# Kernel optimization log

Measured on AMD Instinct MI355X. Metric: run time of the kernel, lower is better.

Reference implementation:

```python
import jax, jax.numpy as jnp
import numpy as np

B, S, A, H1, H2, N = 32768, 512, 8, 400, 300, 3
P = 0.1          # dropout_p
NOISE_VAR = 1e-4  # _noise_variance
INV_SQRT2 = 0.7071067811865476
INV_SQRT2PI = 0.3989422804014327


def adf_relu(m, v):
    # ADF ReLU moment matching (Gast & Roth style, as in adf.ReLU)
    std = jnp.sqrt(v)
    r = m / std
    cdf = 0.5 * (1.0 + jax.lax.erf(r * INV_SQRT2))
    pdf = INV_SQRT2PI * jnp.exp(-0.5 * r * r)
    om = m * cdf + std * pdf
    ov = (m * m + v) * cdf + m * std * pdf - om * om
    return om, ov


def setup_inputs():
    key = jax.random.key(0)
    ks = jax.random.split(key, 10)
    x = jax.random.normal(ks[0], (B, S), jnp.float32)
    x_noise = jax.random.normal(ks[1], (B, S), jnp.float32)
    v1 = 10.0 / np.sqrt(S)   # fanin_init for linear1
    W1 = jax.random.uniform(ks[2], (H1, S), jnp.float32, -v1, v1)
    b1 = jax.random.uniform(ks[3], (H1,), jnp.float32, -1.0 / np.sqrt(S), 1.0 / np.sqrt(S))
    v2 = 10.0 / np.sqrt(H1)  # fanin_init for linear2
    W2 = jax.random.uniform(ks[4], (H2, H1), jnp.float32, -v2, v2)
    b2 = jax.random.uniform(ks[5], (H2,), jnp.float32, -1.0 / np.sqrt(H1), 1.0 / np.sqrt(H1))
    W3 = jax.random.uniform(ks[6], (A, H2), jnp.float32, -0.003, 0.003)
    b3 = jax.random.uniform(ks[7], (A,), jnp.float32, -0.003, 0.003)
    # MC-dropout masks for dropout_n=3 iterations, values in {0, 1/(1-p)}
    mask1 = jax.random.bernoulli(ks[8], 1.0 - P, (N, B, H1)).astype(jnp.float32) / (1.0 - P)
    mask2 = jax.random.bernoulli(ks[9], 1.0 - P, (N, B, H2)).astype(jnp.float32) / (1.0 - P)
    return dict(x=x, x_noise=x_noise, W1=W1, b1=b1, W2=W2, b2=b2, W3=W3, b3=b3,
                mask1=mask1, mask2=mask2)


def reference(x, x_noise, W1, b1, W2, b2, W3, b3, mask1, mask2):
    # input variance: _noise_variance + 2 (constant)
    var0 = jnp.full_like(x, NOISE_VAR + 2.0)
    # global min-max normalize mean, then +0.1
    mn = (x - x.min()) / (x.max() - x.min()) + 0.1
    # linear1 + ADF ReLU are deterministic: compute once, broadcast to N samples
    m = mn @ W1.T + b1              # [B,H1]
    v = var0 @ (W1 * W1).T          # [B,H1]
    m, v = adf_relu(m, v)
    m = m[None] * mask1             # [N,B,H1]
    v = v[None] * (mask1 * mask1)
    m = m @ W2.T + b2               # [N,B,H2]
    v = v @ (W2 * W2).T
    m, v = adf_relu(m, v)
    m = m * mask2
    v = v * (mask2 * mask2)
    m = m @ W3.T + b3               # [N,B,A]
    v = v @ (W3 * W3).T
    mean_out = m.mean(0)            # [B,A]
    # mean of ADF variances + empirical variance of MC means
    var_out = v.mean(0) + ((mean_out[None] - m) ** 2).mean(0)
    var_out = 10.0 ** var_out       # elementwise math.pow(10, .)
    return mean_out, var_out
```

## Files before the change

kernel.cpp:

```cpp
#include <hip/hip_runtime.h>


typedef unsigned short u16;
typedef unsigned int u32;
typedef float f32x4 __attribute__((ext_vector_type(4)));
typedef __bf16 bf16x8 __attribute__((ext_vector_type(8)));
typedef u32 u32x4 __attribute__((ext_vector_type(4)));

union U4 { u32x4 u; bf16x8 v; u16 s[8]; };

#define MFMA16(a, b, c) __builtin_amdgcn_mfma_f32_16x16x32_bf16(a, b, c, 0, 0, 0)

#define B_N 32768
#define S_N 512
#define H1_N 400
#define H2_N 300
#define A_N 8

__device__ __forceinline__ float bf2f(u16 h) {
    union { float f; u32 u; } c; c.u = ((u32)h) << 16; return c.f;
}
__device__ __forceinline__ u16 f2bfbits(float f) {
    union { __bf16 h; u16 u; } c; c.h = (__bf16)f; return c.u;
}
__device__ __forceinline__ u32 encf(float f) {
    u32 u = __float_as_uint(f);
    return (u & 0x80000000u) ? ~u : (u | 0x80000000u);
}
__device__ __forceinline__ float decf(u32 e) {
    u32 u = (e >> 31) ? (e & 0x7FFFFFFFu) : ~e;
    return __uint_as_float(u);
}

__device__ __forceinline__ void adf_relu(float m, float v, float& om, float& ov) {
    v = fmaxf(v, 1e-12f);
    float rstd = rsqrtf(v);
    float stdv = v * rstd;
    float r = m * rstd;
    float e = __expf(-0.5f * r * r);
    float ar = fabsf(r) * 0.70710678118654752f;
    float t = __builtin_amdgcn_rcpf(fmaf(0.3275911f, ar, 1.0f));
    float poly = t * (0.254829592f + t * (-0.284496736f + t * (1.421413741f +
                  t * (-1.453152027f + t * 1.061405429f))));
    float erfa = 1.0f - poly * e;
    float erfv = (r < 0.0f) ? -erfa : erfa;
    float cdf = 0.5f * (1.0f + erfv);
    float pdf = 0.3989422804014327f * e;
    om = fmaf(m, cdf, stdv * pdf);
    ov = fmaf(m * m + v, cdf, m * stdv * pdf) - om * om;
    ov = fmaxf(ov, 0.0f);
}

#define WS_CTL    0u
#define WS_B1F    64u
#define WS_B2F    1664u
#define WS_B3F    2880u
#define WS_RS1    2944u
#define WS_VC1    4544u
#define WS_W3M    6144u
#define WS_W3V    16384u
#define WS_W2SQ   26624u
#define WS_W2B    266624u
#define WS_W1B    506624u
#define WS_OMOV   916224u
#define WS_MP     53345024u
#define WS_VP     56490752u

__global__ void k_detect(const u32* __restrict__ xw, u32* __restrict__ ctl) {
    if (threadIdx.x == 0) {
        int votes = 0;
        for (int i = 0; i < 64; ++i) {
            u32 u = xw[i * 997];
            u32 e = (u >> 7) & 0xFFu;
            votes += (e >= 100u && e <= 145u) ? 1 : 0;
        }
        ctl[0] = (votes >= 40) ? 1u : 0u;
        ctl[1] = 0xFFFFFFFFu;
        ctl[2] = 0u;
    }
}

__global__ void k_weights(const void* __restrict__ w1r, const void* __restrict__ w2r,
                          const void* __restrict__ w3r, const void* __restrict__ b1r,
                          const void* __restrict__ b2r, const void* __restrict__ b3r,
                          const u32* __restrict__ ctl,
                          u16* __restrict__ w1b, u16* __restrict__ w2b,
                          u16* __restrict__ w2sq, u16* __restrict__ w3m,
                          u16* __restrict__ w3v, float* __restrict__ b1f,
                          float* __restrict__ b2f, float* __restrict__ b3f) {
    const bool bf = ctl[0] != 0u;
    const int t = blockIdx.x * 256 + threadIdx.x;

    if (t < (H2_N * H1_N / 8)) {
        float f[8];
        if (bf) {
            U4 d; d.u = *(const u32x4*)((const u16*)w2r + (size_t)t * 8);
            #pragma unroll
            for (int j = 0; j < 8; ++j) f[j] = bf2f(d.s[j]);
        } else {
            f32x4 a = *((const f32x4*)w2r + (size_t)t * 2);
            f32x4 b = *((const f32x4*)w2r + (size_t)t * 2 + 1);
            #pragma unroll
            for (int j = 0; j < 4; ++j) { f[j] = a[j]; f[4 + j] = b[j]; }
        }
        u16 sq[8], cv[8];
        #pragma unroll
        for (int j = 0; j < 8; ++j) { sq[j] = f2bfbits(f[j] * f[j]); cv[j] = f2bfbits(f[j]); }
        *(u32x4*)(w2sq + (size_t)t * 8) = *(u32x4*)sq;
        if (!bf) *(u32x4*)(w2b + (size_t)t * 8) = *(u32x4*)cv;
    }
    if (!bf && t < (H1_N * S_N / 8)) {
        f32x4 a = *((const f32x4*)w1r + (size_t)t * 2);
        f32x4 b = *((const f32x4*)w1r + (size_t)t * 2 + 1);
        u16 cv[8];
        #pragma unroll
        for (int j = 0; j < 4; ++j) { cv[j] = f2bfbits(a[j]); cv[4 + j] = f2bfbits(b[j]); }
        *(u32x4*)(w1b + (size_t)t * 8) = *(u32x4*)cv;
    }
    if (t < 16 * 320) {
        int col = t / 320, k = t - col * 320;
        float f = 0.0f;
        if (col < A_N && k < H2_N)
            f = bf ? bf2f(((const u16*)w3r)[col * H2_N + k]) : ((const float*)w3r)[col * H2_N + k];
        w3m[t] = f2bfbits(f);
        w3v[t] = f2bfbits(f * f);
    }
    if (t < H1_N) b1f[t] = bf ? bf2f(((const u16*)b1r)[t]) : ((const float*)b1r)[t];
    if (t < H2_N) b2f[t] = bf ? bf2f(((const u16*)b2r)[t]) : ((const float*)b2r)[t];
    if (t < A_N)  b3f[t] = bf ? bf2f(((const u16*)b3r)[t]) : ((const float*)b3r)[t];
}

__global__ void k_minmax(const void* __restrict__ xr, u32* __restrict__ ctl) {
    const int tid = threadIdx.x, lane = tid & 63, wv = tid >> 6;
    const bool bf = ctl[0] != 0u;
    float mn = 3.0e38f, mx = -3.0e38f;
    const int idx = blockIdx.x * 256 + tid;
    if (bf) {
        const u16* xg = (const u16*)xr;
        for (int i = idx; i < (B_N * S_N / 8); i += 2048 * 256) {
            U4 d; d.u = *(const u32x4*)(xg + (size_t)i * 8);
            #pragma unroll
            for (int j = 0; j < 8; ++j) {
                float f = bf2f(d.s[j]);
                mn = fminf(mn, f); mx = fmaxf(mx, f);
            }
        }
    } else {
        const f32x4* xf = (const f32x4*)xr;
        for (int i = idx; i < (B_N * S_N / 4); i += 2048 * 256) {
            f32x4 d = xf[i];
            #pragma unroll
            for (int j = 0; j < 4; ++j) {
                mn = fminf(mn, d[j]); mx = fmaxf(mx, d[j]);
            }
        }
    }
    #pragma unroll
    for (int off = 32; off >= 1; off >>= 1) {
        mn = fminf(mn, __shfl_xor(mn, off));
        mx = fmaxf(mx, __shfl_xor(mx, off));
    }
    __shared__ float rmn[4], rmx[4];
    if (lane == 0) { rmn[wv] = mn; rmx[wv] = mx; }
    __syncthreads();
    if (tid == 0) {
        for (int w = 1; w < 4; ++w) { mn = fminf(mn, rmn[w]); mx = fmaxf(mx, rmx[w]); }
        atomicMin(&ctl[1], encf(mn));
        atomicMax(&ctl[2], encf(mx));
    }
}

__global__ void k_prep(const void* __restrict__ w1r, const u32* __restrict__ ctl,
                       float* __restrict__ rs1, float* __restrict__ vc1) {
    const bool bf = ctl[0] != 0u;
    const int h = blockIdx.x, lane = threadIdx.x;
    float f[8];
    if (bf) {
        U4 d; d.u = *(const u32x4*)((const u16*)w1r + (size_t)h * S_N + lane * 8);
        #pragma unroll
        for (int j = 0; j < 8; ++j) f[j] = bf2f(d.s[j]);
    } else {
        f32x4 a = *((const f32x4*)w1r + (size_t)h * 128 + lane * 2);
        f32x4 b = *((const f32x4*)w1r + (size_t)h * 128 + lane * 2 + 1);
        #pragma unroll
        for (int j = 0; j < 4; ++j) { f[j] = a[j]; f[4 + j] = b[j]; }
    }
    float s1 = 0.f, s2 = 0.f;
    #pragma unroll
    for (int j = 0; j < 8; ++j) { s1 += f[j]; s2 += f[j] * f[j]; }
    #pragma unroll
    for (int off = 32; off >= 1; off >>= 1) {
        s1 += __shfl_xor(s1, off);
        s2 += __shfl_xor(s2, off);
    }
    if (lane == 0) { rs1[h] = s1; vc1[h] = 2.0001f * s2; }
}

__global__ __launch_bounds__(256, 4)
void k_l1(const void* __restrict__ xr, const u16* __restrict__ w1bf,
          const u16* __restrict__ w1cv, const float* __restrict__ b1f,
          const float* __restrict__ rs1, const float* __restrict__ vc1,
          const u32* __restrict__ ctl, u32* __restrict__ omovg) {
    const int tid = threadIdx.x, wv = tid >> 6, lane = tid & 63;
    const int lrow = lane & 15, lgrp = lane >> 4;
    const int m0 = blockIdx.x * 128;
    const int n0 = blockIdx.y * 112;
    const bool bf = ctl[0] != 0u;
    const u16* w1 = bf ? w1bf : w1cv;
    const float xmin = decf(ctl[1]), xmax = decf(ctl[2]);
    const float inv = 1.0f / (xmax - xmin);
    const float csh = 0.1f - xmin * inv;

    const f32x4 fz = {0.f, 0.f, 0.f, 0.f};
    f32x4 acc[2][7];
    #pragma unroll
    for (int i = 0; i < 2; ++i)
        #pragma unroll
        for (int j = 0; j < 7; ++j) acc[i][j] = fz;

    const int rowA = m0 + wv * 32 + lrow;
    if (bf) {
        const u16* xg = (const u16*)xr;
        const size_t ar0 = (size_t)rowA * S_N + lgrp * 8;
        const size_t ar1 = ar0 + (size_t)16 * S_N;
        U4 nx0, nx1;
        nx0.u = *(const u32x4*)(xg + ar0);
        nx1.u = *(const u32x4*)(xg + ar1);
        for (int ks = 0; ks < 16; ++ks) {
            U4 a0 = nx0, a1 = nx1;
            if (ks < 15) {
                nx0.u = *(const u32x4*)(xg + ar0 + (ks + 1) * 32);
                nx1.u = *(const u32x4*)(xg + ar1 + (ks + 1) * 32);
            }
            const int k = ks * 32 + lgrp * 8;
            #pragma unroll
            for (int ct = 0; ct < 7; ++ct) {
                const int col = n0 + ct * 16 + lrow;
                U4 b; b.u = 0;
                if (col < H1_N) b.u = *(const u32x4*)(w1 + (size_t)col * S_N + k);
                acc[0][ct] = MFMA16(a0.v, b.v, acc[0][ct]);
                acc[1][ct] = MFMA16(a1.v, b.v, acc[1][ct]);
            }
        }
    } else {
        const f32x4* xf = (const f32x4*)xr;
        const size_t q0 = ((size_t)rowA * S_N + lgrp * 8) >> 2;
        const size_t q1 = q0 + (size_t)16 * S_N / 4;
        f32x4 n0a = xf[q0], n0b = xf[q0 + 1], n1a = xf[q1], n1b = xf[q1 + 1];
        for (int ks = 0; ks < 16; ++ks) {
            f32x4 c0a = n0a, c0b = n0b, c1a = n1a, c1b = n1b;
            if (ks < 15) {
                const size_t o = (size_t)(ks + 1) * 8;
                n0a = xf[q0 + o]; n0b = xf[q0 + o + 1];
                n1a = xf[q1 + o]; n1b = xf[q1 + o + 1];
            }
            U4 a0, a1;
            #pragma unroll
            for (int j = 0; j < 4; ++j) {
                a0.s[j] = f2bfbits(c0a[j]); a0.s[4 + j] = f2bfbits(c0b[j]);
                a1.s[j] = f2bfbits(c1a[j]); a1.s[4 + j] = f2bfbits(c1b[j]);
            }
            const int k = ks * 32 + lgrp * 8;
            #pragma unroll
            for (int ct = 0; ct < 7; ++ct) {
                const int col = n0 + ct * 16 + lrow;
                U4 b; b.u = 0;
                if (col < H1_N) b.u = *(const u32x4*)(w1 + (size_t)col * S_N + k);
                acc[0][ct] = MFMA16(a0.v, b.v, acc[0][ct]);
                acc[1][ct] = MFMA16(a1.v, b.v, acc[1][ct]);
            }
        }
    }
    #pragma unroll
    for (int ct = 0; ct < 7; ++ct) {
        const int col = n0 + ct * 16 + lrow;
        if (col < H1_N) {
            const float c1 = csh * rs1[col] + b1f[col];
            const float vv = vc1[col];
            #pragma unroll
            for (int r2 = 0; r2 < 2; ++r2)
                #pragma unroll
                for (int r = 0; r < 4; ++r) {
                    const int row = m0 + wv * 32 + r2 * 16 + lgrp * 4 + r;
                    float mm = fmaf(inv, acc[r2][ct][r], c1);
                    float omx, ovx; adf_relu(mm, vv, omx, ovx);
                    omovg[(size_t)row * H1_N + col] =
                        (u32)f2bfbits(omx) | ((u32)f2bfbits(ovx) << 16);
                }
        }
    }
}

__global__ __launch_bounds__(256, 3)
void k_l23(const u32* __restrict__ omovg, const u16* __restrict__ w2bf,
           const u16* __restrict__ w2cv, const u16* __restrict__ w2sqg,
           const void* __restrict__ m1r, const void* __restrict__ m2r,
           const float* __restrict__ b2f,
           const u16* __restrict__ w3mg, const u16* __restrict__ w3vg,
           const u32* __restrict__ ctl, float* __restrict__ mpart,
           float* __restrict__ vpart) {
    __shared__ __align__(16) unsigned char smem[52224];
    u16* pmS = (u16*)smem;
    u16* pvS = (u16*)(smem + 26112);
    u16* m2s = (u16*)smem;
    u16* v2s = (u16*)(smem + 26112);

    const int tid = threadIdx.x;
    const int wv = tid >> 6, lane = tid & 63;
    const int lrow = lane & 15, lgrp = lane >> 4;
    const int bx = blockIdx.x;
    const int n = bx % 3;
    const int m0 = (bx / 3) * 32;
    const bool bf = ctl[0] != 0u;
    const u16* w2 = bf ? w2bf : w2cv;
    const f32x4 fz = {0.f, 0.f, 0.f, 0.f};

    #pragma unroll 2
    for (int p = 0; p < 7; ++p) {
        const int c = tid + p * 256;
        if (c < 1600) {
            const int row = c / 50, kc = (c - row * 50) * 8;
            const size_t base = (size_t)(m0 + row) * H1_N + kc;
            u32x4 o0 = *(const u32x4*)(omovg + base);
            u32x4 o1 = *(const u32x4*)(omovg + base + 4);
            const size_t mb = ((size_t)n * B_N + m0 + row) * H1_N + kc;
            u32x4 k0 = {0, 0, 0, 0}, k1 = {0, 0, 0, 0};
            if (bf) {
                k0 = *(const u32x4*)((const u16*)m1r + mb);
            } else {
                k0 = *(const u32x4*)((const float*)m1r + mb);
                k1 = *(const u32x4*)((const float*)m1r + mb + 4);
            }
            u16 pm[8], pv[8];
            #pragma unroll
            for (int j = 0; j < 8; ++j) {
                const u32 w = (j < 4) ? o0[j] : o1[j - 4];
                const float omf = __uint_as_float(w << 16);
                const float ovf = __uint_as_float(w & 0xFFFF0000u);
                float mf;
                if (bf) {
                    const u32 mw = k0[j >> 1];
                    mf = bf2f((u16)((j & 1) ? (mw >> 16) : (mw & 0xFFFFu)));
                } else {
                    mf = __uint_as_float((j < 4) ? k0[j] : k1[j - 4]);
                }
                pm[j] = f2bfbits(omf * mf);
                pv[j] = f2bfbits(ovf * mf * mf);
            }
            *(u32x4*)(pmS + row * 408 + kc) = *(u32x4*)pm;
            *(u32x4*)(pvS + row * 408 + kc) = *(u32x4*)pv;
        }
    }
    __syncthreads();

    f32x4 accM[2][5], accV[2][5];
    #pragma unroll
    for (int i = 0; i < 2; ++i)
        #pragma unroll
        for (int j = 0; j < 5; ++j) { accM[i][j] = fz; accV[i][j] = fz; }

    #pragma unroll 1
    for (int ks = 0; ks < 12; ++ks) {
        const int k0 = ks * 32;
        bf16x8 amf[2], avf[2];
        #pragma unroll
        for (int r2 = 0; r2 < 2; ++r2) {
            const int idx = (r2 * 16 + lrow) * 408 + k0 + lgrp * 8;
            amf[r2] = *(const bf16x8*)(pmS + idx);
            avf[r2] = *(const bf16x8*)(pvS + idx);
        }
        const int kb = k0 + lgrp * 8;
        #pragma unroll
        for (int ct = 0; ct < 5; ++ct) {
            const int col = wv * 80 + ct * 16 + lrow;
            U4 bm, bv; bm.u = 0; bv.u = 0;
            if (col < H2_N) {
                const size_t bidx = (size_t)col * H1_N + kb;
                bm.u = *(const u32x4*)(w2 + bidx);
                bv.u = *(const u32x4*)(w2sqg + bidx);
            }
            accM[0][ct] = MFMA16(amf[0], bm.v, accM[0][ct]);
            accM[1][ct] = MFMA16(amf[1], bm.v, accM[1][ct]);
            accV[0][ct] = MFMA16(avf[0], bv.v, accV[0][ct]);
            accV[1][ct] = MFMA16(avf[1], bv.v, accV[1][ct]);
        }
    }
    {
        const bool kv = lgrp < 2;
        const int ko = kv ? lgrp * 8 : 0;
        bf16x8 amf[2], avf[2];
        #pragma unroll
        for (int r2 = 0; r2 < 2; ++r2) {
            const int idx = (r2 * 16 + lrow) * 408 + 384 + ko;
            U4 ta, tv;
            ta.v = *(const bf16x8*)(pmS + idx);
            tv.v = *(const bf16x8*)(pvS + idx);
            if (!kv) { ta.u = 0; tv.u = 0; }
            amf[r2] = ta.v; avf[r2] = tv.v;
        }
        const int kb = 384 + lgrp * 8;
        #pragma unroll
        for (int ct = 0; ct < 5; ++ct) {
            const int col = wv * 80 + ct * 16 + lrow;
            U4 bm, bv; bm.u = 0; bv.u = 0;
            if (col < H2_N && kb < H1_N) {
                const size_t bidx = (size_t)col * H1_N + kb;
                bm.u = *(const u32x4*)(w2 + bidx);
                bv.u = *(const u32x4*)(w2sqg + bidx);
            }
            accM[0][ct] = MFMA16(amf[0], bm.v, accM[0][ct]);
            accM[1][ct] = MFMA16(amf[1], bm.v, accM[1][ct]);
            accV[0][ct] = MFMA16(avf[0], bv.v, accV[0][ct]);
            accV[1][ct] = MFMA16(avf[1], bv.v, accV[1][ct]);
        }
    }
    __syncthreads();

    float msk[2][5][4];
    #pragma unroll
    for (int r2 = 0; r2 < 2; ++r2)
        #pragma unroll
        for (int ct = 0; ct < 5; ++ct) {
            const int col = wv * 80 + ct * 16 + lrow;
            #pragma unroll
            for (int r = 0; r < 4; ++r) {
                const int rl = r2 * 16 + lgrp * 4 + r;
                float mf = 0.0f;
                if (col < H2_N) {
                    const size_t midx = ((size_t)n * B_N + m0 + rl) * H2_N + col;
                    mf = bf ? bf2f(((const u16*)m2r)[midx])
                            : ((const float*)m2r)[midx];
                }
                msk[r2][ct][r] = mf;
            }
        }

    #pragma unroll
    for (int r2 = 0; r2 < 2; ++r2)
        #pragma unroll
        for (int ct = 0; ct < 5; ++ct) {
            const int col = wv * 80 + ct * 16 + lrow;
            const float b2v = (col < H2_N) ? b2f[col] : 0.0f;
            #pragma unroll
            for (int r = 0; r < 4; ++r) {
                const int rl = r2 * 16 + lgrp * 4 + r;
                u16 wm = 0, wvs = 0;
                if (col < H2_N) {
                    float mm = accM[r2][ct][r] + b2v;
                    float vvx = accV[r2][ct][r];
                    float omx, ovx; adf_relu(mm, vvx, omx, ovx);
                    const float mskv = msk[r2][ct][r];
                    wm  = f2bfbits(omx * mskv);
                    wvs = f2bfbits(ovx * mskv * mskv);
                }
                m2s[rl * 328 + col] = wm;
                v2s[rl * 328 + col] = wvs;
            }
        }
    __syncthreads();

    {
        const int typ = wv & 1, rt = wv >> 1;
        const u16* slab = typ ? v2s : m2s;
        const u16* w3t  = typ ? w3vg : w3mg;
        f32x4 c3 = fz;
        #pragma unroll
        for (int kk = 0; kk < 10; ++kk) {
            const int aidx = (rt * 16 + lrow) * 328 + kk * 32 + lgrp * 8;
            bf16x8 af = *(const bf16x8*)(slab + aidx);
            U4 bw; bw.u = *(const u32x4*)(w3t + (size_t)lrow * 320 + kk * 32 + lgrp * 8);
            c3 = MFMA16(af, bw.v, c3);
        }
        float* part = typ ? vpart : mpart;
        if (lrow < A_N) {
            #pragma unroll
            for (int r = 0; r < 4; ++r) {
                const int rl = rt * 16 + lgrp * 4 + r;
                part[((size_t)n * B_N + m0 + rl) * 8 + lrow] = c3[r];
            }
        }
    }
}

__global__ __launch_bounds__(256)
void k_out(const float* __restrict__ mpart, const float* __restrict__ vpart,
           const float* __restrict__ b3f, const u32* __restrict__ ctl,
           void* __restrict__ outr) {
    const size_t idx = (size_t)blockIdx.x * 256 + threadIdx.x;
    const int a = (int)(idx & 7);
    const size_t st = (size_t)B_N * 8;
    const float m0 = mpart[idx], m1 = mpart[st + idx], m2 = mpart[2 * st + idx];
    const float v0 = vpart[idx], v1 = vpart[st + idx], v2 = vpart[2 * st + idx];
    const float md = (m0 + m1 + m2) * (1.0f / 3.0f);
    const float sm2 = (m0 * m0 + m1 * m1 + m2 * m2) * (1.0f / 3.0f);
    const float meanout = md + b3f[a];
    const float vexp = (v0 + v1 + v2) * (1.0f / 3.0f) + sm2 - md * md;
    const float varout = __expf(vexp * 2.302585092994046f);
    const bool bf = ctl[0] != 0u;
    if (bf) {
        ((u16*)outr)[idx] = f2bfbits(meanout);
        ((u16*)outr)[st + idx] = f2bfbits(varout);
    } else {
        ((float*)outr)[idx] = meanout;
        ((float*)outr)[st + idx] = varout;
    }
}

extern "C" void kernel_launch(void* const* d_in, const int* in_sizes, int n_in,
                              void* d_out, int out_size, void* d_ws, size_t ws_size,
                              hipStream_t stream) {
    const void* x     = d_in[0];
    const void* W1    = d_in[2];
    const void* b1    = d_in[3];
    const void* W2    = d_in[4];
    const void* b2    = d_in[5];
    const void* W3    = d_in[6];
    const void* b3    = d_in[7];
    const void* mask1 = d_in[8];
    const void* mask2 = d_in[9];

    char* ws = (char*)d_ws;
    u32*   ctl   = (u32*)(ws + WS_CTL);
    float* b1f   = (float*)(ws + WS_B1F);
    float* b2f   = (float*)(ws + WS_B2F);
    float* b3f   = (float*)(ws + WS_B3F);
    float* rs1   = (float*)(ws + WS_RS1);
    float* vc1   = (float*)(ws + WS_VC1);
    u16*   w3m   = (u16*)(ws + WS_W3M);
    u16*   w3v   = (u16*)(ws + WS_W3V);
    u16*   w2sq  = (u16*)(ws + WS_W2SQ);
    u16*   w2b   = (u16*)(ws + WS_W2B);
    u16*   w1b   = (u16*)(ws + WS_W1B);
    u32*   omov  = (u32*)(ws + WS_OMOV);
    float* mpart = (float*)(ws + WS_MP);
    float* vpart = (float*)(ws + WS_VP);

    k_detect<<<1, 64, 0, stream>>>((const u32*)x, ctl);
    k_weights<<<100, 256, 0, stream>>>(W1, W2, W3, b1, b2, b3, ctl,
                                       w1b, w2b, w2sq, w3m, w3v, b1f, b2f, b3f);
    k_minmax<<<2048, 256, 0, stream>>>(x, ctl);
    k_prep<<<400, 64, 0, stream>>>(W1, ctl, rs1, vc1);
    k_l1<<<dim3(256, 4), 256, 0, stream>>>(x, (const u16*)W1, w1b, b1f, rs1, vc1,
                                           ctl, omov);
    k_l23<<<3072, 256, 0, stream>>>(omov, (const u16*)W2, w2b, w2sq, mask1, mask2,
                                    b2f, w3m, w3v, ctl, mpart, vpart);
    k_out<<<1024, 256, 0, stream>>>(mpart, vpart, b3f, ctl, d_out);
}
```

Baseline: 658.3 us.

## Compress dropout masks to bitmaps and scale by a single global mask constant

Adds a pre-pass kernel that reads both dropout masks once and packs them into per-element bitmaps. It also ORs all mask bit patterns together to recover the single nonzero scale value. The layer-1 epilogue folds that scale into the stored mean and variance. The layer-2/3 kernel then reads compact bit bytes instead of full float or bf16 masks, replacing the scattered per-element mask2 loads. The OR trick assumes every nonzero mask entry has the same value, and the bitmap path runs only when the workspace is large enough.

```diff
diff --git a/kernel.cpp b/kernel.cpp
--- a/kernel.cpp
+++ b/kernel.cpp
@@ -6,6 +6,7 @@
 typedef float f32x4 __attribute__((ext_vector_type(4)));
 typedef __bf16 bf16x8 __attribute__((ext_vector_type(8)));
 typedef u32 u32x4 __attribute__((ext_vector_type(4)));
+typedef u32 u32x2 __attribute__((ext_vector_type(2)));
 
 union U4 { u32x4 u; bf16x8 v; u16 s[8]; };
 
@@ -65,6 +66,8 @@
 #define WS_OMOV   916224u
 #define WS_MP     53345024u
 #define WS_VP     56490752u
+#define WS_BM1    59636480u
+#define WS_BM2    64551680u
 
 __global__ void k_detect(const u32* __restrict__ xw, u32* __restrict__ ctl) {
     if (threadIdx.x == 0) {
@@ -77,6 +80,94 @@
         ctl[0] = (votes >= 40) ? 1u : 0u;
         ctl[1] = 0xFFFFFFFFu;
         ctl[2] = 0u;
+        ctl[3] = 0u;
+        ctl[4] = 0u;
+    }
+}
+
+__global__ __launch_bounds__(256)
+void k_mcomp(const void* __restrict__ m1r, const void* __restrict__ m2r,
+             u32* __restrict__ ctl, unsigned char* __restrict__ bm1,
+             unsigned char* __restrict__ bm2) {
+    const bool bf = ctl[0] != 0u;
+    const int bid = blockIdx.x;
+    u32 orv = 0;
+    if (bid < 2400) {
+        const int t = bid * 256 + threadIdx.x;
+        const size_t e0 = (size_t)t * 64;
+        u32 b0 = 0, b1 = 0;
+        if (bf) {
+            #pragma unroll
+            for (int v = 0; v < 8; ++v) {
+                u32x4 d = *(const u32x4*)((const u16*)m1r + e0 + v * 8);
+                #pragma unroll
+                for (int j = 0; j < 4; ++j) {
+                    const u32 w = d[j];
+                    orv |= (w << 16) | (w & 0xFFFF0000u);
+                    const int e = v * 8 + j * 2;
+                    if (w & 0xFFFFu) { if (e < 32) b0 |= 1u << e; else b1 |= 1u << (e - 32); }
+                    if (w >> 16) { if (e + 1 < 32) b0 |= 1u << (e + 1); else b1 |= 1u << (e - 31); }
+                }
+            }
+        } else {
+            #pragma unroll
+            for (int v = 0; v < 16; ++v) {
+                u32x4 d = *(const u32x4*)((const u32*)m1r + e0 + v * 4);
+                #pragma unroll
+                for (int j = 0; j < 4; ++j) {
+                    const u32 w = d[j];
+                    orv |= w;
+                    const int e = v * 4 + j;
+                    if (w) { if (e < 32) b0 |= 1u << e; else b1 |= 1u << (e - 32); }
+                }
+            }
+        }
+        u32x2 bb = {b0, b1};
+        *(u32x2*)(bm1 + (size_t)t * 8) = bb;
+        #pragma unroll
+        for (int off = 32; off >= 1; off >>= 1) orv |= __shfl_xor(orv, off);
+        if ((threadIdx.x & 63) == 0 && orv) atomicOr(&ctl[3], orv);
+    } else if (bm2 != nullptr) {
+        const int t = (bid - 2400) * 256 + threadIdx.x;
+        const int row = t / 5, L = t - row * 5;
+        const size_t e0 = (size_t)row * 300 + L * 64;
+        const int nv = (L == 4) ? 11 : 16;
+        u32 b0 = 0, b1 = 0;
+        if (bf) {
+            #pragma unroll
+            for (int v = 0; v < 16; ++v) {
+                if (v < nv) {
+                    u32x2 d = *(const u32x2*)((const u16*)m2r + e0 + v * 4);
+                    #pragma unroll
+                    for (int j = 0; j < 2; ++j) {
+                        const u32 w = d[j];
+                        orv |= (w << 16) | (w & 0xFFFF0000u);
+                        const int e = v * 4 + j * 2;
+                        if (w & 0xFFFFu) { if (e < 32) b0 |= 1u << e; else b1 |= 1u << (e - 32); }
+                        if (w >> 16) { if (e + 1 < 32) b0 |= 1u << (e + 1); else b1 |= 1u << (e - 31); }
+                    }
+                }
+            }
+        } else {
+            #pragma unroll
+            for (int v = 0; v < 16; ++v) {
+                if (v < nv) {
+                    u32x4 d = *(const u32x4*)((const u32*)m2r + e0 + v * 4);
+                    #pragma unroll
+                    for (int j = 0; j < 4; ++j) {
+                        const u32 w = d[j];
+                        orv |= w;
+                        const int e = v * 4 + j;
+                        if (w) { if (e < 32) b0 |= 1u << e; else b1 |= 1u << (e - 32); }
+                    }
+                }
+            }
+        }
+        u32x2 bb = {b0, b1};
+        *(u32x2*)(bm2 + (size_t)row * 40 + L * 8) = bb;
+        #pragma unroll
+        for (int off = 32; off >= 1; off >>= 1) orv |= __shfl_xor(orv, off);
+        if ((threadIdx.x & 63) == 0 && orv) atomicOr(&ctl[4], orv);
     }
 }
 
@@ -200,7 +291,8 @@
 void k_l1(const void* __restrict__ xr, const u16* __restrict__ w1bf,
           const u16* __restrict__ w1cv, const float* __restrict__ b1f,
           const float* __restrict__ rs1, const float* __restrict__ vc1,
-          const u32* __restrict__ ctl, u32* __restrict__ omovg) {
+          const u32* __restrict__ ctl, u32* __restrict__ omovg,
+          const int use_bm1) {
     const int tid = threadIdx.x, wv = tid >> 6, lane = tid & 63;
     const int lrow = lane & 15, lgrp = lane >> 4;
     const int m0 = blockIdx.x * 128;
@@ -210,6 +302,8 @@
     const float xmin = decf(ctl[1]), xmax = decf(ctl[2]);
     const float inv = 1.0f / (xmax - xmin);
     const float csh = 0.1f - xmin * inv;
+    const float c1 = use_bm1 ? __uint_as_float(ctl[3]) : 1.0f;
+    const float c1s = c1 * c1;
 
     const f32x4 fz = {0.f, 0.f, 0.f, 0.f};
     f32x4 acc[2][7];
@@ -275,17 +369,17 @@
     for (int ct = 0; ct < 7; ++ct) {
         const int col = n0 + ct * 16 + lrow;
         if (col < H1_N) {
-            const float c1 = csh * rs1[col] + b1f[col];
+            const float c1b = csh * rs1[col] + b1f[col];
             const float vv = vc1[col];
             #pragma unroll
             for (int r2 = 0; r2 < 2; ++r2)
                 #pragma unroll
                 for (int r = 0; r < 4; ++r) {
                     const int row = m0 + wv * 32 + r2 * 16 + lgrp * 4 + r;
-                    float mm = fmaf(inv, acc[r2][ct][r], c1);
+                    float mm = fmaf(inv, acc[r2][ct][r], c1b);
                     float omx, ovx; adf_relu(mm, vv, omx, ovx);
                     omovg[(size_t)row * H1_N + col] =
-                        (u32)f2bfbits(omx) | ((u32)f2bfbits(ovx) << 16);
+                        (u32)f2bfbits(omx * c1) | ((u32)f2bfbits(ovx * c1s) << 16);
                 }
         }
     }
@@ -298,7 +392,10 @@
            const float* __restrict__ b2f,
            const u16* __restrict__ w3mg, const u16* __restrict__ w3vg,
            const u32* __restrict__ ctl, float* __restrict__ mpart,
-           float* __restrict__ vpart) {
+           float* __restrict__ vpart,
+           const unsigned char* __restrict__ bm1g,
+           const unsigned char* __restrict__ bm2g,
+           const int use_bm1, const int use_bm2) {
     __shared__ __align__(16) unsigned char smem[52224];
     u16* pmS = (u16*)smem;
     u16* pvS = (u16*)(smem + 26112);
@@ -315,40 +412,65 @@
     const u16* w2 = bf ? w2bf : w2cv;
     const f32x4 fz = {0.f, 0.f, 0.f, 0.f};
 
-    #pragma unroll 2
-    for (int p = 0; p < 7; ++p) {
-        const int c = tid + p * 256;
-        if (c < 1600) {
-            const int row = c / 50, kc = (c - row * 50) * 8;
-            const size_t base = (size_t)(m0 + row) * H1_N + kc;
-            u32x4 o0 = *(const u32x4*)(omovg + base);
-            u32x4 o1 = *(const u32x4*)(omovg + base + 4);
-            const size_t mb = ((size_t)n * B_N + m0 + row) * H1_N + kc;
-            u32x4 k0 = {0, 0, 0, 0}, k1 = {0, 0, 0, 0};
-            if (bf) {
-                k0 = *(const u32x4*)((const u16*)m1r + mb);
-            } else {
-                k0 = *(const u32x4*)((const float*)m1r + mb);
-                k1 = *(const u32x4*)((const float*)m1r + mb + 4);
-            }
-            u16 pm[8], pv[8];
-            #pragma unroll
-            for (int j = 0; j < 8; ++j) {
-                const u32 w = (j < 4) ? o0[j] : o1[j - 4];
-                const float omf = __uint_as_float(w << 16);
-                const float ovf = __uint_as_float(w & 0xFFFF0000u);
-                float mf;
+    if (use_bm1) {
+        const unsigned char* brow = bm1g + (size_t)(n * B_N + m0) * 50;
+        #pragma unroll 2
+        for (int p = 0; p < 7; ++p) {
+            const int c = tid + p * 256;
+            if (c < 1600) {
+                const int row = c / 50, kc = (c - row * 50) * 8;
+                const size_t base = (size_t)(m0 + row) * H1_N + kc;
+                u32x4 o0 = *(const u32x4*)(omovg + base);
+                u32x4 o1 = *(const u32x4*)(omovg + base + 4);
+                const unsigned int byte = brow[c];
+                u16 pm[8], pv[8];
+                #pragma unroll
+                for (int j = 0; j < 8; ++j) {
+                    const u32 w = (j < 4) ? o0[j] : o1[j - 4];
+                    const bool bit = (byte >> j) & 1u;
+                    pm[j] = bit ? (u16)(w & 0xFFFFu) : (u16)0;
+                    pv[j] = bit ? (u16)(w >> 16) : (u16)0;
+                }
+                *(u32x4*)(pmS + row * 408 + kc) = *(u32x4*)pm;
+                *(u32x4*)(pvS + row * 408 + kc) = *(u32x4*)pv;
+            }
+        }
+    } else {
+        #pragma unroll 2
+        for (int p = 0; p < 7; ++p) {
+            const int c = tid + p * 256;
+            if (c < 1600) {
+                const int row = c / 50, kc = (c - row * 50) * 8;
+                const size_t base = (size_t)(m0 + row) * H1_N + kc;
+                u32x4 o0 = *(const u32x4*)(omovg + base);
+                u32x4 o1 = *(const u32x4*)(omovg + base + 4);
+                const size_t mb = ((size_t)n * B_N + m0 + row) * H1_N + kc;
+                u32x4 k0 = {0, 0, 0, 0}, k1 = {0, 0, 0, 0};
                 if (bf) {
-                    const u32 mw = k0[j >> 1];
-                    mf = bf2f((u16)((j & 1) ? (mw >> 16) : (mw & 0xFFFFu)));
+                    k0 = *(const u32x4*)((const u16*)m1r + mb);
                 } else {
-                    mf = __uint_as_float((j < 4) ? k0[j] : k1[j - 4]);
-                }
-                pm[j] = f2bfbits(omf * mf);
-                pv[j] = f2bfbits(ovf * mf * mf);
-            }
-            *(u32x4*)(pmS + row * 408 + kc) = *(u32x4*)pm;
-            *(u32x4*)(pvS + row * 408 + kc) = *(u32x4*)pv;
+                    k0 = *(const u32x4*)((const float*)m1r + mb);
+                    k1 = *(const u32x4*)((const float*)m1r + mb + 4);
+                }
+                u16 pm[8], pv[8];
+                #pragma unroll
+                for (int j = 0; j < 8; ++j) {
+                    const u32 w = (j < 4) ? o0[j] : o1[j - 4];
+                    const float omf = __uint_as_float(w << 16);
+                    const float ovf = __uint_as_float(w & 0xFFFF0000u);
+                    float mf;
+                    if (bf) {
+                        const u32 mw = k0[j >> 1];
+                        mf = bf2f((u16)((j & 1) ? (mw >> 16) : (mw & 0xFFFFu)));
+                    } else {
+                        mf = __uint_as_float((j < 4) ? k0[j] : k1[j - 4]);
+                    }
+                    pm[j] = f2bfbits(omf * mf);
+                    pv[j] = f2bfbits(ovf * mf * mf);
+                }
+                *(u32x4*)(pmS + row * 408 + kc) = *(u32x4*)pm;
+                *(u32x4*)(pvS + row * 408 + kc) = *(u32x4*)pv;
+            }
         }
     }
     __syncthreads();
@@ -417,23 +539,40 @@
     __syncthreads();
 
     float msk[2][5][4];
-    #pragma unroll
-    for (int r2 = 0; r2 < 2; ++r2)
+    if (use_bm2) {
+        const float c2 = __uint_as_float(ctl[4]);
+        const unsigned char* brow = bm2g + (size_t)(n * B_N + m0) * 40;
         #pragma unroll
         for (int ct = 0; ct < 5; ++ct) {
             const int col = wv * 80 + ct * 16 + lrow;
             #pragma unroll
-            for (int r = 0; r < 4; ++r) {
-                const int rl = r2 * 16 + lgrp * 4 + r;
-                float mf = 0.0f;
-                if (col < H2_N) {
-                    const size_t midx = ((size_t)n * B_N + m0 + rl) * H2_N + col;
-                    mf = bf ? bf2f(((const u16*)m2r)[midx])
-                            : ((const float*)m2r)[midx];
-                }
-                msk[r2][ct][r] = mf;
-            }
-        }
+            for (int r2 = 0; r2 < 2; ++r2)
+                #pragma unroll
+                for (int r = 0; r < 4; ++r) {
+                    const int rl = r2 * 16 + lgrp * 4 + r;
+                    const unsigned int byte = brow[(size_t)rl * 40 + (col >> 3)];
+                    msk[r2][ct][r] = ((byte >> (col & 7)) & 1u) ? c2 : 0.0f;
+                }
+        }
+    } else {
+        #pragma unroll
+        for (int r2 = 0; r2 < 2; ++r2)
+            #pragma unroll
+            for (int ct = 0; ct < 5; ++ct) {
+                const int col = wv * 80 + ct * 16 + lrow;
+                #pragma unroll
+                for (int r = 0; r < 4; ++r) {
+                    const int rl = r2 * 16 + lgrp * 4 + r;
+                    float mf = 0.0f;
+                    if (col < H2_N) {
+                        const size_t midx = ((size_t)n * B_N + m0 + rl) * H2_N + col;
+                        mf = bf ? bf2f(((const u16*)m2r)[midx])
+                                : ((const float*)m2r)[midx];
+                    }
+                    msk[r2][ct][r] = mf;
+                }
+            }
+    }
 
     #pragma unroll
     for (int r2 = 0; r2 < 2; ++r2)
@@ -534,15 +673,24 @@
     u32*   omov  = (u32*)(ws + WS_OMOV);
     float* mpart = (float*)(ws + WS_MP);
     float* vpart = (float*)(ws + WS_VP);
+    unsigned char* bm1 = (unsigned char*)(ws + WS_BM1);
+    unsigned char* bm2 = (unsigned char*)(ws + WS_BM2);
+
+    const int use_bm1 = (ws_size >= (size_t)WS_BM1 + 4915200u) ? 1 : 0;
+    const int use_bm2 = (ws_size >= (size_t)WS_BM2 + 3932160u) ? 1 : 0;
 
     k_detect<<<1, 64, 0, stream>>>((const u32*)x, ctl);
+    if (use_bm1)
+        k_mcomp<<<use_bm2 ? 4320 : 2400, 256, 0, stream>>>(
+            mask1, mask2, ctl, bm1, use_bm2 ? bm2 : (unsigned char*)nullptr);
     k_weights<<<100, 256, 0, stream>>>(W1, W2, W3, b1, b2, b3, ctl,
                                        w1b, w2b, w2sq, w3m, w3v, b1f, b2f, b3f);
     k_minmax<<<2048, 256, 0, stream>>>(x, ctl);
     k_prep<<<400, 64, 0, stream>>>(W1, ctl, rs1, vc1);
     k_l1<<<dim3(256, 4), 256, 0, stream>>>(x, (const u16*)W1, w1b, b1f, rs1, vc1,
-                                           ctl, omov);
+                                           ctl, omov, use_bm1);
     k_l23<<<3072, 256, 0, stream>>>(omov, (const u16*)W2, w2b, w2sq, mask1, mask2,
-                                    b2f, w3m, w3v, ctl, mpart, vpart);
+                                    b2f, w3m, w3v, ctl, mpart, vpart,
+                                    bm1, bm2, use_bm1, use_bm2);
     k_out<<<1024, 256, 0, stream>>>(mpart, vpart, b3f, ctl, d_out);
 }
```

Result: slower. 820.9 us (+24.7%).
